# Optimization experiments

Measured on AMD Instinct MI355X. Metric: run time of the kernel, lower is better.

The kernel has to match this reference:

```python
import jax, jax.numpy as jnp
import numpy as np

DEGREE = 3
NUM_POINTS = 1024
EPS = 1e-5


def jacobi_kan(x, coeffs, a=1.0, b=1.0, degree=DEGREE):
    # x: (B, C_in, N) -> y: (B, C_out, N)
    t = jnp.tanh(jnp.transpose(x, (0, 2, 1)))  # (B, N, C_in)
    polys = [jnp.ones_like(t)]
    if degree > 0:
        polys.append((a - b + (a + b + 2.0) * t) / 2.0)
    for i in range(2, degree + 1):
        A = (2 * i + a + b - 1) * (2 * i + a + b) / (2 * i * (i + a + b))
        B = (2 * i + a + b - 1) * (a ** 2 - b ** 2) / (2 * i * (i + a + b) * (2 * i + a + b - 2))
        C = -2 * (i + a - 1) * (i + b - 1) * (2 * i + a + b) / (2 * i * (i + a + b) * (2 * i + a + b - 2))
        polys.append((A * t + B) * polys[-1] + C * polys[-2])
    jac = jnp.stack(polys, axis=-1)  # (B, N, C_in, D+1)
    return jnp.einsum('bnid,iod->bon', jac, coeffs)


def batchnorm(x):
    # x: (B, C, N); training-mode BN with batch stats, gamma=1, beta=0
    m = jnp.mean(x, axis=(0, 2), keepdims=True)
    v = jnp.var(x, axis=(0, 2), keepdims=True)
    return (x - m) * jax.lax.rsqrt(v + EPS)


def setup_inputs() -> dict:
    key = jax.random.key(0)
    ks = jax.random.split(key, 11)
    dims = [(2, 64), (64, 64), (64, 64), (64, 128), (128, 1024),
            (1088, 512), (512, 256), (256, 128), (128, 128), (128, 3)]
    inp = {"x": jax.random.normal(ks[0], (32, 2, NUM_POINTS), dtype=jnp.float32)}
    for idx, (i, o) in enumerate(dims):
        std = 1.0 / (i * (DEGREE + 1))
        inp[f"w{idx+1}"] = std * jax.random.normal(ks[idx + 1], (i, o, DEGREE + 1), dtype=jnp.float32)
    return inp


def reference(x, w1, w2, w3, w4, w5, w6, w7, w8, w9, w10):
    h = batchnorm(jacobi_kan(x, w1))
    h = batchnorm(jacobi_kan(h, w2))
    local_feature = h                                  # (B, 64, N)
    h = batchnorm(jacobi_kan(h, w3))
    h = batchnorm(jacobi_kan(h, w4))
    h = batchnorm(jacobi_kan(h, w5))                   # (B, 1024, N)
    gf = jnp.max(h, axis=2, keepdims=True)             # (B, 1024, 1)
    gf = jnp.broadcast_to(gf, (h.shape[0], h.shape[1], NUM_POINTS))
    h = jnp.concatenate([local_feature, gf], axis=1)   # (B, 1088, N)
    h = batchnorm(jacobi_kan(h, w6))
    h = batchnorm(jacobi_kan(h, w7))
    h = batchnorm(jacobi_kan(h, w8))
    h = batchnorm(jacobi_kan(h, w9))
    return jacobi_kan(h, w10)                          # (B, 3, N)
```

## Files before the change

### kernel.cpp

```cpp
#include <hip/hip_runtime.h>

#define BATCH 32
#define NPTS  1024
#define NTOT  (BATCH * NPTS)

typedef _Float16 half8  __attribute__((ext_vector_type(8)));
typedef _Float16 half4v __attribute__((ext_vector_type(4)));
typedef float    f32x4  __attribute__((ext_vector_type(4)));


__device__ __forceinline__ float fast_tanh(float x) {
  float ax = fabsf(x);
  float e  = __expf(-2.0f * ax);
  float t  = (1.0f - e) / (1.0f + e);
  return x < 0.0f ? -t : t;
}

__device__ __forceinline__ void jacobi4(float t, float& p0, float& p1, float& p2, float& p3) {
  float t2 = t * t;
  p0 = 1.0f;
  p1 = 2.0f * t;
  p2 = 3.75f * t2 - 0.75f;
  p3 = t * (7.0f * t2 - 3.0f);
}

__device__ __forceinline__ unsigned encf(float f) {
  unsigned b = __float_as_uint(f);
  return b ^ ((unsigned)((int)b >> 31) | 0x80000000u);
}
__device__ __forceinline__ float decf(unsigned u) {
  unsigned b = (u & 0x80000000u) ? (u ^ 0x80000000u) : ~u;
  return __uint_as_float(b);
}

__global__ void zero_ws(unsigned* __restrict__ p, int n) {
  int i = blockIdx.x * 256 + threadIdx.x;
  if (i < n) p[i] = 0u;
}

__global__ void conv_w16(const float* __restrict__ w, half8* __restrict__ wh,
                         int C_in, int C_out, int BN) {
  const int nslot = C_in >> 1;
  int tid = blockIdx.x * 256 + threadIdx.x;
  int oL = tid % BN;
  int r  = tid / BN;
  int s  = r % nslot;
  int ot = r / nslot;
  int i  = s << 1;
  int o  = ot * BN + oL;
  const float4 wa = *(const float4*)(w + (((size_t)i * C_out + o) << 2));
  const float4 wb = *(const float4*)(w + (((size_t)(i + 1) * C_out + o) << 2));
  half8 h;
  h[0] = (_Float16)(wa.x * 64.0f); h[1] = (_Float16)(wa.y * 64.0f);
  h[2] = (_Float16)(wa.z * 64.0f); h[3] = (_Float16)(wa.w * 64.0f);
  h[4] = (_Float16)(wb.x * 64.0f); h[5] = (_Float16)(wb.y * 64.0f);
  h[6] = (_Float16)(wb.z * 64.0f); h[7] = (_Float16)(wb.w * 64.0f);
  wh[tid] = h;
}

__global__ __launch_bounds__(256) void act_tanh(
    float* y, const float2* __restrict__ st, int C)
{
  size_t i = (((size_t)blockIdx.x << 8) + threadIdx.x) << 2;
  int c = (int)((i >> 10) % (unsigned)C);
  float2 s = st[c];
  float4 v = *(float4*)(y + i);
  v.x = fast_tanh((v.x - s.x) * s.y);
  v.y = fast_tanh((v.y - s.x) * s.y);
  v.z = fast_tanh((v.z - s.x) * s.y);
  v.w = fast_tanh((v.w - s.x) * s.y);
  *(float4*)(y + i) = v;
}

template<int NBW>
__global__ __launch_bounds__(NBW * 128, 2) void kan_mfma3(
    const float* __restrict__ T,
    const half8* __restrict__ wh,
    const float* __restrict__ bias,
    float*       __restrict__ out,
    float2*      __restrict__ spart,
    float*       __restrict__ stat_acc,
    unsigned*    __restrict__ max_acc,
    int C_in, int C_out)
{
  constexpr int BN = NBW * 64;
  const int nslot = C_in >> 1;
  __shared__ float sredS[BN][2], sredS2[BN][2], sredM[BN][2];

  const int t    = threadIdx.x;
  const int lane = t & 63;
  const int col  = lane & 15;
  const int quad = lane >> 4;
  const int wv   = t >> 6;
  const int wm   = wv & 1;
  const int wn   = wv >> 1;
  const int b    = blockIdx.x >> 3;
  const int n0   = (blockIdx.x & 7) << 7;
  const int o0   = blockIdx.y * BN;

  f32x4 acc[4][4];
#pragma unroll
  for (int i = 0; i < 4; ++i)
#pragma unroll
    for (int j = 0; j < 4; ++j)
#pragma unroll
      for (int k = 0; k < 4; ++k) acc[i][j][k] = 0.0f;

  const float* Tp = T + (((size_t)(b * C_in + (quad << 1))) << 10) + n0 + (wm << 6) + col;
  const half8* Bp = wh + (size_t)blockIdx.y * nslot * BN + (size_t)quad * BN + wn * 64 + col;

  for (int s4 = 0; s4 < nslot; s4 += 4) {
    float t0[4], t1[4];
    half8 bf[4];
#pragma unroll
    for (int f = 0; f < 4; ++f) {
      t0[f] = Tp[f << 4];
      t1[f] = Tp[(f << 4) + 1024];
      bf[f] = Bp[f << 4];
    }
    Tp += (size_t)8 << 10;
    Bp += (size_t)4 * BN;
    half8 af[4];
#pragma unroll
    for (int f = 0; f < 4; ++f) {
      float a = t0[f], c = t1[f];
      float as = a * a, cs = c * c;
      half8 h;
      h[0] = (_Float16)1.0f;
      h[1] = (_Float16)(a + a);
      h[2] = (_Float16)(3.75f * as - 0.75f);
      h[3] = (_Float16)(a * (7.0f * as - 3.0f));
      h[4] = (_Float16)1.0f;
      h[5] = (_Float16)(c + c);
      h[6] = (_Float16)(3.75f * cs - 0.75f);
      h[7] = (_Float16)(c * (7.0f * cs - 3.0f));
      af[f] = h;
    }
#pragma unroll
    for (int fm = 0; fm < 4; ++fm)
#pragma unroll
      for (int fn = 0; fn < 4; ++fn)
        acc[fm][fn] = __builtin_amdgcn_mfma_f32_16x16x32_f16(af[fm], bf[fn], acc[fm][fn], 0, 0, 0);
  }

  const float inv64 = 0.015625f;
#pragma unroll
  for (int fn = 0; fn < 4; ++fn) {
    const int cl = (wn << 6) + (fn << 4) + col;
    const int o  = o0 + cl;
    const float bb = bias ? bias[b * C_out + o] : 0.0f;
    float s = 0.f, s2 = 0.f, mx = -3.4e38f;
#pragma unroll
    for (int fm = 0; fm < 4; ++fm) {
      float v0 = acc[fm][fn][0] * inv64 + bb;
      float v1 = acc[fm][fn][1] * inv64 + bb;
      float v2 = acc[fm][fn][2] * inv64 + bb;
      float v3 = acc[fm][fn][3] * inv64 + bb;
      if (out) {
        *(float4*)(out + (((size_t)(b * C_out + o)) << 10) + n0 + (wm << 6) + (fm << 4) + (quad << 2)) =
            make_float4(v0, v1, v2, v3);
      }
      s  += v0 + v1 + v2 + v3;
      s2 += v0 * v0 + v1 * v1 + v2 * v2 + v3 * v3;
      mx  = fmaxf(fmaxf(v0, v1), fmaxf(fmaxf(v2, v3), mx));
    }
    s  += __shfl_down(s, 32);  s  += __shfl_down(s, 16);
    s2 += __shfl_down(s2, 32); s2 += __shfl_down(s2, 16);
    mx  = fmaxf(mx, __shfl_down(mx, 32)); mx = fmaxf(mx, __shfl_down(mx, 16));
    if (lane < 16) {
      sredS [cl][wm] = s;
      sredS2[cl][wm] = s2;
      sredM [cl][wm] = mx;
    }
  }
  __syncthreads();
  if (t < BN) {
    const int o = o0 + t;
    float s  = sredS [t][0] + sredS [t][1];
    float s2 = sredS2[t][0] + sredS2[t][1];
    if (out) {
      spart[(o << 8) + blockIdx.x] = make_float2(s, s2);
    } else {
      float mx = fmaxf(sredM[t][0], sredM[t][1]);
      atomicAdd(&stat_acc[o], s);
      atomicAdd(&stat_acc[C_out + o], s2);
      atomicMax(&max_acc[b * C_out + o], encf(mx));
    }
  }
}

template<int BM, int BN>
__global__ __launch_bounds__(256) void kan_gemm(
    const float*  __restrict__ in, const float2* __restrict__ stats,
    const float*  __restrict__ w, float* __restrict__ out,
    float2* __restrict__ spart, int C_in, int C_out)
{
  static_assert(BM * BN == 256 * 64, "8x8-per-thread tile requires BM*BN == 16384");
  constexpr int TM = BM / 8;
  constexpr int AE = 8 * BM / 256;
  constexpr int BE = 8 * BN / 256;
  __shared__ __align__(16) float As[32][BM];
  __shared__ __align__(16) float Bs[32][BN];

  const int t  = threadIdx.x;
  const int tpb = NPTS / BM;
  const int b  = blockIdx.x / tpb;
  const int n0 = (blockIdx.x % tpb) * BM;
  const int o0 = blockIdx.y * BN;
  const int tm = t % TM;
  const int to = t / TM;

  float acc[2][4][2][4];
#pragma unroll
  for (int a = 0; a < 2; ++a)
#pragma unroll
    for (int c = 0; c < 4; ++c)
#pragma unroll
      for (int d = 0; d < 2; ++d)
#pragma unroll
        for (int e = 0; e < 4; ++e) acc[a][c][d][e] = 0.0f;

  const int nch = (C_in + 7) >> 3;
  for (int ch = 0; ch < nch; ++ch) {
    const int i0 = ch << 3;
    __syncthreads();
#pragma unroll
    for (int r = 0; r < AE; ++r) {
      int e  = t + (r << 8);
      int il = e / BM, n = e % BM;
      int i  = i0 + il;
      float p0 = 0.f, p1 = 0.f, p2 = 0.f, p3 = 0.f;
      if (i < C_in) {
        float v = in[((size_t)(b * C_in + i) << 10) + n0 + n];
        if (stats) { float2 s = stats[i]; v = (v - s.x) * s.y; }
        jacobi4(fast_tanh(v), p0, p1, p2, p3);
      }
      As[(il << 2) + 0][n] = p0;
      As[(il << 2) + 1][n] = p1;
      As[(il << 2) + 2][n] = p2;
      As[(il << 2) + 3][n] = p3;
    }
#pragma unroll
    for (int r = 0; r < BE; ++r) {
      int e  = t + (r << 8);
      int il = e / BN, o = e % BN;
      int i  = i0 + il;
      float4 wv = make_float4(0.f, 0.f, 0.f, 0.f);
      if (i < C_in) wv = *(const float4*)(w + (((size_t)i * C_out + o0 + o) << 2));
      Bs[(il << 2) + 0][o] = wv.x;
      Bs[(il << 2) + 1][o] = wv.y;
      Bs[(il << 2) + 2][o] = wv.z;
      Bs[(il << 2) + 3][o] = wv.w;
    }
    __syncthreads();
#pragma unroll 8
    for (int k = 0; k < 32; ++k) {
      const float4 a0 = *(const float4*)&As[k][tm << 2];
      const float4 a1 = *(const float4*)&As[k][(BM / 2) + (tm << 2)];
      const float4 b0 = *(const float4*)&Bs[k][to << 2];
      const float4 b1 = *(const float4*)&Bs[k][(BN / 2) + (to << 2)];
      const float am[2][4] = {{a0.x, a0.y, a0.z, a0.w}, {a1.x, a1.y, a1.z, a1.w}};
      const float bo[2][4] = {{b0.x, b0.y, b0.z, b0.w}, {b1.x, b1.y, b1.z, b1.w}};
#pragma unroll
      for (int oh = 0; oh < 2; ++oh)
#pragma unroll
        for (int oj = 0; oj < 4; ++oj) {
          const float bv = bo[oh][oj];
#pragma unroll
          for (int mh = 0; mh < 2; ++mh)
#pragma unroll
            for (int mj = 0; mj < 4; ++mj)
              acc[oh][oj][mh][mj] = fmaf(bv, am[mh][mj], acc[oh][oj][mh][mj]);
        }
    }
  }

#pragma unroll
  for (int oh = 0; oh < 2; ++oh)
#pragma unroll
    for (int oj = 0; oj < 4; ++oj) {
      const int o = o0 + oh * (BN / 2) + (to << 2) + oj;
      float s = 0.f, s2 = 0.f;
#pragma unroll
      for (int mh = 0; mh < 2; ++mh) {
        float4 v = make_float4(acc[oh][oj][mh][0], acc[oh][oj][mh][1],
                               acc[oh][oj][mh][2], acc[oh][oj][mh][3]);
        *(float4*)(out + (((size_t)(b * C_out + o)) << 10) + n0 + mh * (BM / 2) + (tm << 2)) = v;
        s  += v.x + v.y + v.z + v.w;
        s2 += v.x * v.x + v.y * v.y + v.z * v.z + v.w * v.w;
      }
#pragma unroll
      for (int off = TM / 2; off > 0; off >>= 1) {
        s  += __shfl_down(s, off, TM);
        s2 += __shfl_down(s2, off, TM);
      }
      if (tm == 0) spart[(o << 8) + blockIdx.x] = make_float2(s, s2);
    }
}

__global__ __launch_bounds__(256) void bn_finalize2(
    const float2* __restrict__ spart, float2* __restrict__ stats, int C, int nxb)
{
  int c = blockIdx.x, t = threadIdx.x;
  float s = 0.f, s2 = 0.f;
  if (t < nxb) { float2 p = spart[(c << 8) + t]; s = p.x; s2 = p.y; }
#pragma unroll
  for (int off = 32; off > 0; off >>= 1) {
    s  += __shfl_down(s, off);
    s2 += __shfl_down(s2, off);
  }
  __shared__ float rs[4], rs2[4];
  int wid = t >> 6;
  if ((t & 63) == 0) { rs[wid] = s; rs2[wid] = s2; }
  __syncthreads();
  if (t == 0) {
    s  = rs[0] + rs[1] + rs[2] + rs[3];
    s2 = rs2[0] + rs2[1] + rs2[2] + rs2[3];
    float m   = s * (1.0f / NTOT);
    float var = s2 * (1.0f / NTOT) - m * m;
    stats[c] = make_float2(m, rsqrtf(var + 1e-5f));
  }
}

__global__ void bn_finalize(const float* __restrict__ stat_acc,
                            float2* __restrict__ stats, int C) {
  int c = blockIdx.x * 256 + threadIdx.x;
  if (c < C) {
    float m   = stat_acc[c] * (1.0f / NTOT);
    float var = stat_acc[C + c] * (1.0f / NTOT) - m * m;
    stats[c] = make_float2(m, rsqrtf(var + 1e-5f));
  }
}

__global__ __launch_bounds__(256) void pool_const6p(
    const unsigned* __restrict__ max_acc, const float2* __restrict__ stats5,
    const float* __restrict__ w6, float* __restrict__ cst)
{
  __shared__ __align__(16) float4 P[32][64];
  const int t  = threadIdx.x;
  const int ot = blockIdx.x;
  const int c0 = blockIdx.y << 6;
#pragma unroll
  for (int it = 0; it < 8; ++it) {
    int idx = t + (it << 8);
    int b = idx >> 6, cl = idx & 63;
    int c = c0 + cl;
    float mx = decf(max_acc[(b << 10) + c]);
    float2 s = stats5[c];
    float tt = fast_tanh((mx - s.x) * s.y);
    float p0, p1, p2, p3; jacobi4(tt, p0, p1, p2, p3);
    P[b][cl] = make_float4(p0, p1, p2, p3);
  }
  __syncthreads();
  const int oL = t & 63;
  const int bg = t >> 6;
  const int o  = (ot << 6) + oL;
  float acc[8];
#pragma unroll
  for (int i = 0; i < 8; ++i) acc[i] = 0.f;
  for (int cl = 0; cl < 64; ++cl) {
    const float4 wv = *(const float4*)(w6 + (((size_t)(64 + c0 + cl) * 512 + o) << 2));
#pragma unroll
    for (int bb = 0; bb < 8; ++bb) {
      float4 p = P[(bg << 3) + bb][cl];
      acc[bb] += p.x * wv.x + p.y * wv.y + p.z * wv.z + p.w * wv.w;
    }
  }
#pragma unroll
  for (int bb = 0; bb < 8; ++bb)
    atomicAdd(&cst[(((bg << 3) + bb) << 9) + o], acc[bb]);
}

__global__ __launch_bounds__(256) void kan_final(
    const float* __restrict__ in, const float2* __restrict__ stats,
    const float* __restrict__ w, float* __restrict__ out)
{
  int g = blockIdx.x * 256 + threadIdx.x;
  int b = g >> 10, n = g & 1023;
  float a0 = 0.f, a1 = 0.f, a2 = 0.f;
  for (int i = 0; i < 128; ++i) {
    float v = in[((size_t)(b * 128 + i) << 10) + n];
    float2 s = stats[i];
    float p0, p1, p2, p3; jacobi4(fast_tanh((v - s.x) * s.y), p0, p1, p2, p3);
    const float4 w0 = *(const float4*)(w + ((i * 3 + 0) << 2));
    const float4 w1 = *(const float4*)(w + ((i * 3 + 1) << 2));
    const float4 w2 = *(const float4*)(w + ((i * 3 + 2) << 2));
    a0 += p0 * w0.x + p1 * w0.y + p2 * w0.z + p3 * w0.w;
    a1 += p0 * w1.x + p1 * w1.y + p2 * w1.z + p3 * w1.w;
    a2 += p0 * w2.x + p1 * w2.y + p2 * w2.z + p3 * w2.w;
  }
  out[((b * 3 + 0) << 10) + n] = a0;
  out[((b * 3 + 1) << 10) + n] = a1;
  out[((b * 3 + 2) << 10) + n] = a2;
}

extern "C" void kernel_launch(void* const* d_in, const int* in_sizes, int n_in,
                              void* d_out, int out_size, void* d_ws, size_t ws_size,
                              hipStream_t stream) {
  const float* x   = (const float*)d_in[0];
  const float* w1  = (const float*)d_in[1];
  const float* w2  = (const float*)d_in[2];
  const float* w3  = (const float*)d_in[3];
  const float* w4  = (const float*)d_in[4];
  const float* w5  = (const float*)d_in[5];
  const float* w6  = (const float*)d_in[6];
  const float* w7  = (const float*)d_in[7];
  const float* w8  = (const float*)d_in[8];
  const float* w9  = (const float*)d_in[9];
  const float* w10 = (const float*)d_in[10];

  float* ws = (float*)d_ws;
  float*    stat_acc = ws + 0;
  unsigned* maxenc   = (unsigned*)(ws + 2048);
  float*    cst6     = ws + 34816;
  float2*   spart    = (float2*)(ws + 51200);
  float2*   stats1   = (float2*)(ws + 313344);
  float2*   stats2   = stats1 + 64;
  float2*   stats3   = stats2 + 64;
  float2*   stats4   = stats3 + 64;
  float2*   stats5   = stats4 + 128;
  float2*   stats6   = stats5 + 1024;
  float2*   stats7   = stats6 + 512;
  float2*   stats8   = stats7 + 256;
  float2*   stats9   = stats8 + 128;
  half8*    whbase = (half8*)(ws + 318464);
  half8*    h2 = whbase + 0;
  half8*    h3 = whbase + 2048;
  half8*    h4 = whbase + 4096;
  half8*    h5 = whbase + 8192;
  half8*    h6 = whbase + 73728;
  half8*    h7 = whbase + 90112;
  half8*    h8 = whbase + 155648;
  half8*    h9 = whbase + 172032;
  float* P   = ws + 1048576;
  float* yT2 = P;
  float* y6  = P + 2097152;
  float* y1  = P + 2097152;
  float* y3  = P + 4194304;
  float* y4  = P + 6291456;
  float* y8  = P + 2097152;
  float* y9  = P + 6291456;
  float* y7  = P + 18874368;

  dim3 blk(256);
  zero_ws<<<200, blk, 0, stream>>>((unsigned*)ws, 51200);
  conv_w16<<<8,   blk, 0, stream>>>(w2, h2, 64, 64, 64);
  conv_w16<<<8,   blk, 0, stream>>>(w3, h3, 64, 64, 64);
  conv_w16<<<16,  blk, 0, stream>>>(w4, h4, 64, 128, 128);
  conv_w16<<<256, blk, 0, stream>>>(w5, h5, 128, 1024, 128);
  conv_w16<<<64,  blk, 0, stream>>>(w6, h6, 64, 512, 128);
  conv_w16<<<256, blk, 0, stream>>>(w7, h7, 512, 256, 128);
  conv_w16<<<64,  blk, 0, stream>>>(w8, h8, 256, 128, 128);
  conv_w16<<<32,  blk, 0, stream>>>(w9, h9, 128, 128, 128);

  kan_gemm<256, 64><<<dim3(128, 1), blk, 0, stream>>>(x, nullptr, w1, y1, spart, 2, 64);
  bn_finalize2<<<64, blk, 0, stream>>>(spart, stats1, 64, 128);
  act_tanh<<<32 * 64, blk, 0, stream>>>(y1, stats1, 64);
  kan_mfma3<1><<<dim3(256, 1), 128, 0, stream>>>(y1, h2, nullptr, yT2, spart, nullptr, nullptr, 64, 64);
  bn_finalize2<<<64, blk, 0, stream>>>(spart, stats2, 64, 256);
  act_tanh<<<32 * 64, blk, 0, stream>>>(yT2, stats2, 64);
  kan_mfma3<1><<<dim3(256, 1), 128, 0, stream>>>(yT2, h3, nullptr, y3, spart, nullptr, nullptr, 64, 64);
  bn_finalize2<<<64, blk, 0, stream>>>(spart, stats3, 64, 256);
  act_tanh<<<32 * 64, blk, 0, stream>>>(y3, stats3, 64);
  kan_mfma3<2><<<dim3(256, 1), blk, 0, stream>>>(y3, h4, nullptr, y4, spart, nullptr, nullptr, 64, 128);
  bn_finalize2<<<128, blk, 0, stream>>>(spart, stats4, 128, 256);
  act_tanh<<<32 * 128, blk, 0, stream>>>(y4, stats4, 128);
  kan_mfma3<2><<<dim3(256, 8), blk, 0, stream>>>(y4, h5, nullptr, nullptr, nullptr, stat_acc, maxenc, 128, 1024);
  bn_finalize<<<4, blk, 0, stream>>>(stat_acc, stats5, 1024);
  pool_const6p<<<dim3(8, 16), blk, 0, stream>>>(maxenc, stats5, w6, cst6);
  kan_mfma3<2><<<dim3(256, 4), blk, 0, stream>>>(yT2, h6, cst6, y6, spart, nullptr, nullptr, 64, 512);
  bn_finalize2<<<512, blk, 0, stream>>>(spart, stats6, 512, 256);
  act_tanh<<<32 * 512, blk, 0, stream>>>(y6, stats6, 512);
  kan_mfma3<2><<<dim3(256, 2), blk, 0, stream>>>(y6, h7, nullptr, y7, spart, nullptr, nullptr, 512, 256);
  bn_finalize2<<<256, blk, 0, stream>>>(spart, stats7, 256, 256);
  act_tanh<<<32 * 256, blk, 0, stream>>>(y7, stats7, 256);
  kan_mfma3<2><<<dim3(256, 1), blk, 0, stream>>>(y7, h8, nullptr, y8, spart, nullptr, nullptr, 256, 128);
  bn_finalize2<<<128, blk, 0, stream>>>(spart, stats8, 128, 256);
  act_tanh<<<32 * 128, blk, 0, stream>>>(y8, stats8, 128);
  kan_mfma3<2><<<dim3(256, 1), blk, 0, stream>>>(y8, h9, nullptr, y9, spart, nullptr, nullptr, 128, 128);
  bn_finalize2<<<128, blk, 0, stream>>>(spart, stats9, 128, 256);
  kan_final<<<128, blk, 0, stream>>>(y9, stats9, w10, (float*)d_out);
}
```

Measured before the change: 422.6 us.

## Precompute fp16 Jacobi basis activations and fold P0 term into per-channel bias

Adds an act_poly3 pass that applies BN plus tanh and writes the P1..P3 Jacobi basis values as packed fp16 in a K-major layout. A new kan_mfma4 GEMM then streams those operands straight into MFMA instead of building them inside the inner loop. The constant P0=1 term is dropped from the GEMM and replaced by a precomputed column sum of w[:, :, 0] added as a bias, which cuts K by a quarter. The tradeoff is an extra fp16 activation buffer written and read per layer, and the new path only runs when the workspace is at least about 189 MB, otherwise the old path is kept.

New measurement: 606.4 us. 1.44x slower.

```diff
diff --git a/kernel.cpp b/kernel.cpp
--- a/kernel.cpp
+++ b/kernel.cpp
@@ -58,6 +58,43 @@
   wh[tid] = h;
 }
 
+__global__ __launch_bounds__(256) void conv_w16_3(
+    const float* __restrict__ w, half8* __restrict__ wh,
+    int C_in, int C_out, int BN)
+{
+  const int C8  = C_in >> 3;
+  const int nK8 = 3 * C8;
+  int tid = blockIdx.x * 256 + threadIdx.x;
+  int oL = tid % BN;
+  int r  = tid / BN;
+  int kg = r % nK8;
+  int ot = r / nK8;
+  int j  = kg / C8;
+  int cb = (kg - j * C8) << 3;
+  int o  = ot * BN + oL;
+  half8 h;
+#pragma unroll
+  for (int e = 0; e < 8; ++e) {
+    float v = w[(((size_t)(cb + e) * C_out + o) << 2) + (j + 1)];
+    h[e] = (_Float16)(v * 64.0f);
+  }
+  wh[tid] = h;
+}
+
+__global__ __launch_bounds__(256) void w0sum(
+    const float* __restrict__ w, float* __restrict__ s, int C_in, int C_out)
+{
+  __shared__ float r[3][64];
+  const int oL  = threadIdx.x & 63;
+  const int seg = threadIdx.x >> 6;
+  const int o   = (blockIdx.x << 6) + oL;
+  float a = 0.f;
+  for (int i = seg; i < C_in; i += 4) a += w[(((size_t)i * C_out + o) << 2)];
+  if (seg) r[seg - 1][oL] = a;
+  __syncthreads();
+  if (seg == 0) s[o] = a + r[0][oL] + r[1][oL] + r[2][oL];
+}
+
 __global__ __launch_bounds__(256) void act_tanh(
     float* y, const float2* __restrict__ st, int C)
 {
@@ -70,6 +107,56 @@
   v.z = fast_tanh((v.z - s.x) * s.y);
   v.w = fast_tanh((v.w - s.x) * s.y);
   *(float4*)(y + i) = v;
+}
+
+__global__ __launch_bounds__(256) void act_poly3(
+    const float* __restrict__ y, const float2* __restrict__ st,
+    half8* __restrict__ A, int C)
+{
+  const int C8 = C >> 3;
+  const int b  = blockIdx.x / C8;
+  const int cg = blockIdx.x - b * C8;
+  const int n  = threadIdx.x << 2;
+  const float* yp = y + (((size_t)(b * C + (cg << 3))) << 10) + n;
+  float q1[8][4], q2[8][4], q3[8][4];
+#pragma unroll
+  for (int e = 0; e < 8; ++e) {
+    float2 s = st[(cg << 3) + e];
+    float4 v = *(const float4*)(yp + ((size_t)e << 10));
+    float tv[4] = {v.x, v.y, v.z, v.w};
+#pragma unroll
+    for (int k = 0; k < 4; ++k) {
+      float tt = fast_tanh((tv[k] - s.x) * s.y);
+      float t2 = tt * tt;
+      q1[e][k] = tt + tt;
+      q2[e][k] = 3.75f * t2 - 0.75f;
+      q3[e][k] = tt * (7.0f * t2 - 3.0f);
+    }
+  }
+  half8* Ap = A + (((size_t)(b * 3 * C8 + cg)) << 10) + n;
+#pragma unroll
+  for (int k = 0; k < 4; ++k) {
+    half8 h;
+#pragma unroll
+    for (int e = 0; e < 8; ++e) h[e] = (_Float16)q1[e][k];
+    Ap[k] = h;
+  }
+  Ap += (size_t)C8 << 10;
+#pragma unroll
+  for (int k = 0; k < 4; ++k) {
+    half8 h;
+#pragma unroll
+    for (int e = 0; e < 8; ++e) h[e] = (_Float16)q2[e][k];
+    Ap[k] = h;
+  }
+  Ap += (size_t)C8 << 10;
+#pragma unroll
+  for (int k = 0; k < 4; ++k) {
+    half8 h;
+#pragma unroll
+    for (int e = 0; e < 8; ++e) h[e] = (_Float16)q3[e][k];
+    Ap[k] = h;
+  }
 }
 
 template<int NBW>
@@ -149,6 +236,105 @@
     const int cl = (wn << 6) + (fn << 4) + col;
     const int o  = o0 + cl;
     const float bb = bias ? bias[b * C_out + o] : 0.0f;
+    float s = 0.f, s2 = 0.f, mx = -3.4e38f;
+#pragma unroll
+    for (int fm = 0; fm < 4; ++fm) {
+      float v0 = acc[fm][fn][0] * inv64 + bb;
+      float v1 = acc[fm][fn][1] * inv64 + bb;
+      float v2 = acc[fm][fn][2] * inv64 + bb;
+      float v3 = acc[fm][fn][3] * inv64 + bb;
+      if (out) {
+        *(float4*)(out + (((size_t)(b * C_out + o)) << 10) + n0 + (wm << 6) + (fm << 4) + (quad << 2)) =
+            make_float4(v0, v1, v2, v3);
+      }
+      s  += v0 + v1 + v2 + v3;
+      s2 += v0 * v0 + v1 * v1 + v2 * v2 + v3 * v3;
+      mx  = fmaxf(fmaxf(v0, v1), fmaxf(fmaxf(v2, v3), mx));
+    }
+    s  += __shfl_down(s, 32);  s  += __shfl_down(s, 16);
+    s2 += __shfl_down(s2, 32); s2 += __shfl_down(s2, 16);
+    mx  = fmaxf(mx, __shfl_down(mx, 32)); mx = fmaxf(mx, __shfl_down(mx, 16));
+    if (lane < 16) {
+      sredS [cl][wm] = s;
+      sredS2[cl][wm] = s2;
+      sredM [cl][wm] = mx;
+    }
+  }
+  __syncthreads();
+  if (t < BN) {
+    const int o = o0 + t;
+    float s  = sredS [t][0] + sredS [t][1];
+    float s2 = sredS2[t][0] + sredS2[t][1];
+    if (out) {
+      spart[(o << 8) + blockIdx.x] = make_float2(s, s2);
+    } else {
+      float mx = fmaxf(sredM[t][0], sredM[t][1]);
+      atomicAdd(&stat_acc[o], s);
+      atomicAdd(&stat_acc[C_out + o], s2);
+      atomicMax(&max_acc[b * C_out + o], encf(mx));
+    }
+  }
+}
+
+template<int NBW>
+__global__ __launch_bounds__(NBW * 128, 2) void kan_mfma4(
+    const half8* __restrict__ A,
+    const half8* __restrict__ wh,
+    const float* __restrict__ w0s,
+    const float* __restrict__ bias,
+    float*       __restrict__ out,
+    float2*      __restrict__ spart,
+    float*       __restrict__ stat_acc,
+    unsigned*    __restrict__ max_acc,
+    int nK8, int C_out)
+{
+  constexpr int BN = NBW * 64;
+  __shared__ float sredS[BN][2], sredS2[BN][2], sredM[BN][2];
+
+  const int t    = threadIdx.x;
+  const int lane = t & 63;
+  const int col  = lane & 15;
+  const int quad = lane >> 4;
+  const int wv   = t >> 6;
+  const int wm   = wv & 1;
+  const int wn   = wv >> 1;
+  const int b    = blockIdx.x >> 3;
+  const int n0   = (blockIdx.x & 7) << 7;
+  const int o0   = blockIdx.y * BN;
+
+  f32x4 acc[4][4];
+#pragma unroll
+  for (int i = 0; i < 4; ++i)
+#pragma unroll
+    for (int j = 0; j < 4; ++j)
+#pragma unroll
+      for (int k = 0; k < 4; ++k) acc[i][j][k] = 0.0f;
+
+  const half8* Ap = A + (((size_t)b * nK8 + quad) << 10) + n0 + (wm << 6) + col;
+  const half8* Bp = wh + (size_t)blockIdx.y * nK8 * BN + (size_t)quad * BN + wn * 64 + col;
+
+  for (int g = 0; g < nK8; g += 4) {
+    half8 af[4], bf[4];
+#pragma unroll
+    for (int f = 0; f < 4; ++f) {
+      af[f] = Ap[f << 4];
+      bf[f] = Bp[f << 4];
+    }
+    Ap += (size_t)4 << 10;
+    Bp += (size_t)4 * BN;
+#pragma unroll
+    for (int fm = 0; fm < 4; ++fm)
+#pragma unroll
+      for (int fn = 0; fn < 4; ++fn)
+        acc[fm][fn] = __builtin_amdgcn_mfma_f32_16x16x32_f16(af[fm], bf[fn], acc[fm][fn], 0, 0, 0);
+  }
+
+  const float inv64 = 0.015625f;
+#pragma unroll
+  for (int fn = 0; fn < 4; ++fn) {
+    const int cl = (wn << 6) + (fn << 4) + col;
+    const int o  = o0 + cl;
+    const float bb = w0s[o] + (bias ? bias[b * C_out + o] : 0.0f);
     float s = 0.f, s2 = 0.f, mx = -3.4e38f;
 #pragma unroll
     for (int fm = 0; fm < 4; ++fm) {
@@ -410,74 +596,174 @@
   const float* w10 = (const float*)d_in[10];
 
   float* ws = (float*)d_ws;
-  float*    stat_acc = ws + 0;
-  unsigned* maxenc   = (unsigned*)(ws + 2048);
-  float*    cst6     = ws + 34816;
-  float2*   spart    = (float2*)(ws + 51200);
-  float2*   stats1   = (float2*)(ws + 313344);
-  float2*   stats2   = stats1 + 64;
-  float2*   stats3   = stats2 + 64;
-  float2*   stats4   = stats3 + 64;
-  float2*   stats5   = stats4 + 128;
-  float2*   stats6   = stats5 + 1024;
-  float2*   stats7   = stats6 + 512;
-  float2*   stats8   = stats7 + 256;
-  float2*   stats9   = stats8 + 128;
-  half8*    whbase = (half8*)(ws + 318464);
-  half8*    h2 = whbase + 0;
-  half8*    h3 = whbase + 2048;
-  half8*    h4 = whbase + 4096;
-  half8*    h5 = whbase + 8192;
-  half8*    h6 = whbase + 73728;
-  half8*    h7 = whbase + 90112;
-  half8*    h8 = whbase + 155648;
-  half8*    h9 = whbase + 172032;
-  float* P   = ws + 1048576;
-  float* yT2 = P;
-  float* y6  = P + 2097152;
-  float* y1  = P + 2097152;
-  float* y3  = P + 4194304;
-  float* y4  = P + 6291456;
-  float* y8  = P + 2097152;
-  float* y9  = P + 6291456;
-  float* y7  = P + 18874368;
-
   dim3 blk(256);
-  zero_ws<<<200, blk, 0, stream>>>((unsigned*)ws, 51200);
-  conv_w16<<<8,   blk, 0, stream>>>(w2, h2, 64, 64, 64);
-  conv_w16<<<8,   blk, 0, stream>>>(w3, h3, 64, 64, 64);
-  conv_w16<<<16,  blk, 0, stream>>>(w4, h4, 64, 128, 128);
-  conv_w16<<<256, blk, 0, stream>>>(w5, h5, 128, 1024, 128);
-  conv_w16<<<64,  blk, 0, stream>>>(w6, h6, 64, 512, 128);
-  conv_w16<<<256, blk, 0, stream>>>(w7, h7, 512, 256, 128);
-  conv_w16<<<64,  blk, 0, stream>>>(w8, h8, 256, 128, 128);
-  conv_w16<<<32,  blk, 0, stream>>>(w9, h9, 128, 128, 128);
-
-  kan_gemm<256, 64><<<dim3(128, 1), blk, 0, stream>>>(x, nullptr, w1, y1, spart, 2, 64);
-  bn_finalize2<<<64, blk, 0, stream>>>(spart, stats1, 64, 128);
-  act_tanh<<<32 * 64, blk, 0, stream>>>(y1, stats1, 64);
-  kan_mfma3<1><<<dim3(256, 1), 128, 0, stream>>>(y1, h2, nullptr, yT2, spart, nullptr, nullptr, 64, 64);
-  bn_finalize2<<<64, blk, 0, stream>>>(spart, stats2, 64, 256);
-  act_tanh<<<32 * 64, blk, 0, stream>>>(yT2, stats2, 64);
-  kan_mfma3<1><<<dim3(256, 1), 128, 0, stream>>>(yT2, h3, nullptr, y3, spart, nullptr, nullptr, 64, 64);
-  bn_finalize2<<<64, blk, 0, stream>>>(spart, stats3, 64, 256);
-  act_tanh<<<32 * 64, blk, 0, stream>>>(y3, stats3, 64);
-  kan_mfma3<2><<<dim3(256, 1), blk, 0, stream>>>(y3, h4, nullptr, y4, spart, nullptr, nullptr, 64, 128);
-  bn_finalize2<<<128, blk, 0, stream>>>(spart, stats4, 128, 256);
-  act_tanh<<<32 * 128, blk, 0, stream>>>(y4, stats4, 128);
-  kan_mfma3<2><<<dim3(256, 8), blk, 0, stream>>>(y4, h5, nullptr, nullptr, nullptr, stat_acc, maxenc, 128, 1024);
-  bn_finalize<<<4, blk, 0, stream>>>(stat_acc, stats5, 1024);
-  pool_const6p<<<dim3(8, 16), blk, 0, stream>>>(maxenc, stats5, w6, cst6);
-  kan_mfma3<2><<<dim3(256, 4), blk, 0, stream>>>(yT2, h6, cst6, y6, spart, nullptr, nullptr, 64, 512);
-  bn_finalize2<<<512, blk, 0, stream>>>(spart, stats6, 512, 256);
-  act_tanh<<<32 * 512, blk, 0, stream>>>(y6, stats6, 512);
-  kan_mfma3<2><<<dim3(256, 2), blk, 0, stream>>>(y6, h7, nullptr, y7, spart, nullptr, nullptr, 512, 256);
-  bn_finalize2<<<256, blk, 0, stream>>>(spart, stats7, 256, 256);
-  act_tanh<<<32 * 256, blk, 0, stream>>>(y7, stats7, 256);
-  kan_mfma3<2><<<dim3(256, 1), blk, 0, stream>>>(y7, h8, nullptr, y8, spart, nullptr, nullptr, 256, 128);
-  bn_finalize2<<<128, blk, 0, stream>>>(spart, stats8, 128, 256);
-  act_tanh<<<32 * 128, blk, 0, stream>>>(y8, stats8, 128);
-  kan_mfma3<2><<<dim3(256, 1), blk, 0, stream>>>(y8, h9, nullptr, y9, spart, nullptr, nullptr, 128, 128);
-  bn_finalize2<<<128, blk, 0, stream>>>(spart, stats9, 128, 256);
-  kan_final<<<128, blk, 0, stream>>>(y9, stats9, w10, (float*)d_out);
-}
+
+  if (ws_size >= 188743680ULL) {
+    float*    stat_acc = ws + 0;
+    unsigned* maxenc   = (unsigned*)(ws + 2048);
+    float*    cst6     = ws + 34816;
+    float2*   spart    = (float2*)(ws + 51200);
+    float2*   stats1   = (float2*)(ws + 313344);
+    float2*   stats2   = stats1 + 64;
+    float2*   stats3   = stats2 + 64;
+    float2*   stats4   = stats3 + 64;
+    float2*   stats5   = stats4 + 128;
+    float2*   stats6   = stats5 + 1024;
+    float2*   stats7   = stats6 + 512;
+    float2*   stats8   = stats7 + 256;
+    float2*   stats9   = stats8 + 128;
+    float*    w0s2 = ws + 318080;
+    float*    w0s3 = w0s2 + 64;
+    float*    w0s4 = w0s3 + 64;
+    float*    w0s5 = w0s4 + 128;
+    float*    w0s6 = w0s5 + 1024;
+    float*    w0s7 = w0s6 + 512;
+    float*    w0s8 = w0s7 + 256;
+    float*    w0s9 = w0s8 + 128;
+    half8*    whb = (half8*)(ws + 320384);
+    half8*    h2 = whb + 0;
+    half8*    h3 = whb + 1536;
+    half8*    h4 = whb + 3072;
+    half8*    h5 = whb + 6144;
+    half8*    h6 = whb + 55296;
+    half8*    h7 = whb + 67584;
+    half8*    h8 = whb + 116736;
+    half8*    h9 = whb + 129024;
+    const size_t MF = 1048576;
+    float* P  = ws + 2 * MF;
+    float* A2 = P;
+    float* y1 = P + 3 * MF;
+    float* A1 = P + 5 * MF;
+    float* y2 = P + 3 * MF;
+    float* y3 = P + 5 * MF;
+    float* A3 = P + 7 * MF;
+    float* y4 = P + 3 * MF;
+    float* A4 = P + 7 * MF;
+    float* y6 = P + 3 * MF;
+    float* A6 = P + 19 * MF;
+    float* y7 = P;
+    float* A7 = P + 8 * MF;
+    float* y8 = P;
+    float* A8 = P + 4 * MF;
+    float* y9 = P;
+
+    zero_ws<<<200, blk, 0, stream>>>((unsigned*)ws, 51200);
+    conv_w16_3<<<6,   blk, 0, stream>>>(w2, h2, 64, 64, 64);
+    conv_w16_3<<<6,   blk, 0, stream>>>(w3, h3, 64, 64, 64);
+    conv_w16_3<<<12,  blk, 0, stream>>>(w4, h4, 64, 128, 128);
+    conv_w16_3<<<192, blk, 0, stream>>>(w5, h5, 128, 1024, 128);
+    conv_w16_3<<<48,  blk, 0, stream>>>(w6, h6, 64, 512, 128);
+    conv_w16_3<<<192, blk, 0, stream>>>(w7, h7, 512, 256, 128);
+    conv_w16_3<<<48,  blk, 0, stream>>>(w8, h8, 256, 128, 128);
+    conv_w16_3<<<24,  blk, 0, stream>>>(w9, h9, 128, 128, 128);
+    w0sum<<<1,  blk, 0, stream>>>(w2, w0s2, 64, 64);
+    w0sum<<<1,  blk, 0, stream>>>(w3, w0s3, 64, 64);
+    w0sum<<<2,  blk, 0, stream>>>(w4, w0s4, 64, 128);
+    w0sum<<<16, blk, 0, stream>>>(w5, w0s5, 128, 1024);
+    w0sum<<<8,  blk, 0, stream>>>(w6, w0s6, 64, 512);
+    w0sum<<<4,  blk, 0, stream>>>(w7, w0s7, 512, 256);
+    w0sum<<<2,  blk, 0, stream>>>(w8, w0s8, 256, 128);
+    w0sum<<<2,  blk, 0, stream>>>(w9, w0s9, 128, 128);
+
+    kan_gemm<256, 64><<<dim3(128, 1), blk, 0, stream>>>(x, nullptr, w1, y1, spart, 2, 64);
+    bn_finalize2<<<64, blk, 0, stream>>>(spart, stats1, 64, 128);
+    act_poly3<<<256, blk, 0, stream>>>(y1, stats1, (half8*)A1, 64);
+    kan_mfma4<1><<<dim3(256, 1), 128, 0, stream>>>((half8*)A1, h2, w0s2, nullptr, y2, spart, nullptr, nullptr, 24, 64);
+    bn_finalize2<<<64, blk, 0, stream>>>(spart, stats2, 64, 256);
+    act_poly3<<<256, blk, 0, stream>>>(y2, stats2, (half8*)A2, 64);
+    kan_mfma4<1><<<dim3(256, 1), 128, 0, stream>>>((half8*)A2, h3, w0s3, nullptr, y3, spart, nullptr, nullptr, 24, 64);
+    bn_finalize2<<<64, blk, 0, stream>>>(spart, stats3, 64, 256);
+    act_poly3<<<256, blk, 0, stream>>>(y3, stats3, (half8*)A3, 64);
+    kan_mfma4<2><<<dim3(256, 1), blk, 0, stream>>>((half8*)A3, h4, w0s4, nullptr, y4, spart, nullptr, nullptr, 24, 128);
+    bn_finalize2<<<128, blk, 0, stream>>>(spart, stats4, 128, 256);
+    act_poly3<<<512, blk, 0, stream>>>(y4, stats4, (half8*)A4, 128);
+    kan_mfma4<2><<<dim3(256, 8), blk, 0, stream>>>((half8*)A4, h5, w0s5, nullptr, nullptr, nullptr, stat_acc, maxenc, 48, 1024);
+    bn_finalize<<<4, blk, 0, stream>>>(stat_acc, stats5, 1024);
+    pool_const6p<<<dim3(8, 16), blk, 0, stream>>>(maxenc, stats5, w6, cst6);
+    kan_mfma4<2><<<dim3(256, 4), blk, 0, stream>>>((half8*)A2, h6, w0s6, cst6, y6, spart, nullptr, nullptr, 24, 512);
+    bn_finalize2<<<512, blk, 0, stream>>>(spart, stats6, 512, 256);
+    act_poly3<<<2048, blk, 0, stream>>>(y6, stats6, (half8*)A6, 512);
+    kan_mfma4<2><<<dim3(256, 2), blk, 0, stream>>>((half8*)A6, h7, w0s7, nullptr, y7, spart, nullptr, nullptr, 192, 256);
+    bn_finalize2<<<256, blk, 0, stream>>>(spart, stats7, 256, 256);
+    act_poly3<<<1024, blk, 0, stream>>>(y7, stats7, (half8*)A7, 256);
+    kan_mfma4<2><<<dim3(256, 1), blk, 0, stream>>>((half8*)A7, h8, w0s8, nullptr, y8, spart, nullptr, nullptr, 96, 128);
+    bn_finalize2<<<128, blk, 0, stream>>>(spart, stats8, 128, 256);
+    act_poly3<<<512, blk, 0, stream>>>(y8, stats8, (half8*)A8, 128);
+    kan_mfma4<2><<<dim3(256, 1), blk, 0, stream>>>((half8*)A8, h9, w0s9, nullptr, y9, spart, nullptr, nullptr, 48, 128);
+    bn_finalize2<<<128, blk, 0, stream>>>(spart, stats9, 128, 256);
+    kan_final<<<128, blk, 0, stream>>>(y9, stats9, w10, (float*)d_out);
+    return;
+  }
+
+  {
+    float*    stat_acc = ws + 0;
+    unsigned* maxenc   = (unsigned*)(ws + 2048);
+    float*    cst6     = ws + 34816;
+    float2*   spart    = (float2*)(ws + 51200);
+    float2*   stats1   = (float2*)(ws + 313344);
+    float2*   stats2   = stats1 + 64;
+    float2*   stats3   = stats2 + 64;
+    float2*   stats4   = stats3 + 64;
+    float2*   stats5   = stats4 + 128;
+    float2*   stats6   = stats5 + 1024;
+    float2*   stats7   = stats6 + 512;
+    float2*   stats8   = stats7 + 256;
+    float2*   stats9   = stats8 + 128;
+    half8*    whbase = (half8*)(ws + 318464);
+    half8*    h2 = whbase + 0;
+    half8*    h3 = whbase + 2048;
+    half8*    h4 = whbase + 4096;
+    half8*    h5 = whbase + 8192;
+    half8*    h6 = whbase + 73728;
+    half8*    h7 = whbase + 90112;
+    half8*    h8 = whbase + 155648;
+    half8*    h9 = whbase + 172032;
+    float* P   = ws + 1048576;
+    float* yT2 = P;
+    float* y6  = P + 2097152;
+    float* y1  = P + 2097152;
+    float* y3  = P + 4194304;
+    float* y4  = P + 6291456;
+    float* y8  = P + 2097152;
+    float* y9  = P + 6291456;
+    float* y7  = P + 18874368;
+
+    zero_ws<<<200, blk, 0, stream>>>((unsigned*)ws, 51200);
+    conv_w16<<<8,   blk, 0, stream>>>(w2, h2, 64, 64, 64);
+    conv_w16<<<8,   blk, 0, stream>>>(w3, h3, 64, 64, 64);
+    conv_w16<<<16,  blk, 0, stream>>>(w4, h4, 64, 128, 128);
+    conv_w16<<<256, blk, 0, stream>>>(w5, h5, 128, 1024, 128);
+    conv_w16<<<64,  blk, 0, stream>>>(w6, h6, 64, 512, 128);
+    conv_w16<<<256, blk, 0, stream>>>(w7, h7, 512, 256, 128);
+    conv_w16<<<64,  blk, 0, stream>>>(w8, h8, 256, 128, 128);
+    conv_w16<<<32,  blk, 0, stream>>>(w9, h9, 128, 128, 128);
+
+    kan_gemm<256, 64><<<dim3(128, 1), blk, 0, stream>>>(x, nullptr, w1, y1, spart, 2, 64);
+    bn_finalize2<<<64, blk, 0, stream>>>(spart, stats1, 64, 128);
+    act_tanh<<<32 * 64, blk, 0, stream>>>(y1, stats1, 64);
+    kan_mfma3<1><<<dim3(256, 1), 128, 0, stream>>>(y1, h2, nullptr, yT2, spart, nullptr, nullptr, 64, 64);
+    bn_finalize2<<<64, blk, 0, stream>>>(spart, stats2, 64, 256);
+    act_tanh<<<32 * 64, blk, 0, stream>>>(yT2, stats2, 64);
+    kan_mfma3<1><<<dim3(256, 1), 128, 0, stream>>>(yT2, h3, nullptr, y3, spart, nullptr, nullptr, 64, 64);
+    bn_finalize2<<<64, blk, 0, stream>>>(spart, stats3, 64, 256);
+    act_tanh<<<32 * 64, blk, 0, stream>>>(y3, stats3, 64);
+    kan_mfma3<2><<<dim3(256, 1), blk, 0, stream>>>(y3, h4, nullptr, y4, spart, nullptr, nullptr, 64, 128);
+    bn_finalize2<<<128, blk, 0, stream>>>(spart, stats4, 128, 256);
+    act_tanh<<<32 * 128, blk, 0, stream>>>(y4, stats4, 128);
+    kan_mfma3<2><<<dim3(256, 8), blk, 0, stream>>>(y4, h5, nullptr, nullptr, nullptr, stat_acc, maxenc, 128, 1024);
+    bn_finalize<<<4, blk, 0, stream>>>(stat_acc, stats5, 1024);
+    pool_const6p<<<dim3(8, 16), blk, 0, stream>>>(maxenc, stats5, w6, cst6);
+    kan_mfma3<2><<<dim3(256, 4), blk, 0, stream>>>(yT2, h6, cst6, y6, spart, nullptr, nullptr, 64, 512);
+    bn_finalize2<<<512, blk, 0, stream>>>(spart, stats6, 512, 256);
+    act_tanh<<<32 * 512, blk, 0, stream>>>(y6, stats6, 512);
+    kan_mfma3<2><<<dim3(256, 2), blk, 0, stream>>>(y6, h7, nullptr, y7, spart, nullptr, nullptr, 512, 256);
+    bn_finalize2<<<256, blk, 0, stream>>>(spart, stats7, 256, 256);
+    act_tanh<<<32 * 256, blk, 0, stream>>>(y7, stats7, 256);
+    kan_mfma3<2><<<dim3(256, 1), blk, 0, stream>>>(y7, h8, nullptr, y8, spart, nullptr, nullptr, 256, 128);
+    bn_finalize2<<<128, blk, 0, stream>>>(spart, stats8, 128, 256);
+    act_tanh<<<32 * 128, blk, 0, stream>>>(y8, stats8, 128);
+    kan_mfma3<2><<<dim3(256, 1), blk, 0, stream>>>(y8, h9, nullptr, y9, spart, nullptr, nullptr, 128, 128);
+    bn_finalize2<<<128, blk, 0, stream>>>(spart, stats9, 128, 256);
+    kan_final<<<128, blk, 0, stream>>>(y9, stats9, w10, (float*)d_out);
+  }
+}
```

## Store tanh activations as packed fp16 pairs and double-buffer GEMM loads

Applied to the files above, without the earlier changes.

The activation kernel now writes tanh outputs as packed half2 pairs interleaved by channel pair, in a separate buffer rather than in place. The MFMA kernel reads these halved-size operands, computes the Jacobi basis with packed fp16 arithmetic, and software-pipelines its loads with two register buffers. The workspace buffer layout is reorganised to match. This cuts activation-read bandwidth and the conversion ALU work in the GEMMs, at the cost of computing the polynomial basis in fp16, which lowers precision, and more registers for the double buffer.

New measurement: 382.6 us. -9.5%, faster.

```diff
diff --git a/kernel.cpp b/kernel.cpp
--- a/kernel.cpp
+++ b/kernel.cpp
@@ -5,7 +5,7 @@
 #define NTOT  (BATCH * NPTS)
 
 typedef _Float16 half8  __attribute__((ext_vector_type(8)));
-typedef _Float16 half4v __attribute__((ext_vector_type(4)));
+typedef _Float16 half2v __attribute__((ext_vector_type(2)));
 typedef float    f32x4  __attribute__((ext_vector_type(4)));
 
 
@@ -58,23 +58,36 @@
   wh[tid] = h;
 }
 
-__global__ __launch_bounds__(256) void act_tanh(
-    float* y, const float2* __restrict__ st, int C)
+__global__ __launch_bounds__(256) void act_tanh16(
+    const float* __restrict__ y, const float2* __restrict__ st,
+    unsigned* __restrict__ T16, int C)
 {
-  size_t i = (((size_t)blockIdx.x << 8) + threadIdx.x) << 2;
-  int c = (int)((i >> 10) % (unsigned)C);
-  float2 s = st[c];
-  float4 v = *(float4*)(y + i);
-  v.x = fast_tanh((v.x - s.x) * s.y);
-  v.y = fast_tanh((v.y - s.x) * s.y);
-  v.z = fast_tanh((v.z - s.x) * s.y);
-  v.w = fast_tanh((v.w - s.x) * s.y);
-  *(float4*)(y + i) = v;
+  const int nslot = C >> 1;
+  const int b  = blockIdx.x / nslot;
+  const int s  = blockIdx.x - b * nslot;
+  const int n  = threadIdx.x << 2;
+  const float* yp = y + (((size_t)(b * C + (s << 1))) << 10) + n;
+  const float2 s0 = st[(s << 1)];
+  const float2 s1 = st[(s << 1) + 1];
+  float4 v0 = *(const float4*)yp;
+  float4 v1 = *(const float4*)(yp + 1024);
+  float a0[4] = {v0.x, v0.y, v0.z, v0.w};
+  float a1[4] = {v1.x, v1.y, v1.z, v1.w};
+  unsigned r[4];
+#pragma unroll
+  for (int k = 0; k < 4; ++k) {
+    _Float16 h0 = (_Float16)fast_tanh((a0[k] - s0.x) * s0.y);
+    _Float16 h1 = (_Float16)fast_tanh((a1[k] - s1.x) * s1.y);
+    unsigned lo = (unsigned)__builtin_bit_cast(unsigned short, h0);
+    unsigned hi = (unsigned)__builtin_bit_cast(unsigned short, h1);
+    r[k] = lo | (hi << 16);
+  }
+  *(uint4*)(T16 + (((size_t)(b * nslot + s)) << 10) + n) = make_uint4(r[0], r[1], r[2], r[3]);
 }
 
 template<int NBW>
-__global__ __launch_bounds__(NBW * 128, 2) void kan_mfma3(
-    const float* __restrict__ T,
+__global__ __launch_bounds__(NBW * 128, 2) void kan_mfma7(
+    const unsigned* __restrict__ T16,
     const half8* __restrict__ wh,
     const float* __restrict__ bias,
     float*       __restrict__ out,
@@ -106,42 +119,61 @@
 #pragma unroll
       for (int k = 0; k < 4; ++k) acc[i][j][k] = 0.0f;
 
-  const float* Tp = T + (((size_t)(b * C_in + (quad << 1))) << 10) + n0 + (wm << 6) + col;
-  const half8* Bp = wh + (size_t)blockIdx.y * nslot * BN + (size_t)quad * BN + wn * 64 + col;
-
-  for (int s4 = 0; s4 < nslot; s4 += 4) {
-    float t0[4], t1[4];
-    half8 bf[4];
-#pragma unroll
-    for (int f = 0; f < 4; ++f) {
-      t0[f] = Tp[f << 4];
-      t1[f] = Tp[(f << 4) + 1024];
-      bf[f] = Bp[f << 4];
-    }
-    Tp += (size_t)8 << 10;
-    Bp += (size_t)4 * BN;
-    half8 af[4];
-#pragma unroll
-    for (int f = 0; f < 4; ++f) {
-      float a = t0[f], c = t1[f];
-      float as = a * a, cs = c * c;
-      half8 h;
-      h[0] = (_Float16)1.0f;
-      h[1] = (_Float16)(a + a);
-      h[2] = (_Float16)(3.75f * as - 0.75f);
-      h[3] = (_Float16)(a * (7.0f * as - 3.0f));
-      h[4] = (_Float16)1.0f;
-      h[5] = (_Float16)(c + c);
-      h[6] = (_Float16)(3.75f * cs - 0.75f);
-      h[7] = (_Float16)(c * (7.0f * cs - 3.0f));
-      af[f] = h;
-    }
-#pragma unroll
-    for (int fm = 0; fm < 4; ++fm)
-#pragma unroll
-      for (int fn = 0; fn < 4; ++fn)
-        acc[fm][fn] = __builtin_amdgcn_mfma_f32_16x16x32_f16(af[fm], bf[fn], acc[fm][fn], 0, 0, 0);
-  }
+  const unsigned* Tp = T16 + (((size_t)(b * nslot + quad)) << 10) + n0 + (wm << 6) + col;
+  const half8*    Bp = wh + (size_t)blockIdx.y * nslot * BN + (size_t)quad * BN + wn * 64 + col;
+
+  const half2v c375  = {(_Float16)3.75f,  (_Float16)3.75f};
+  const half2v cm075 = {(_Float16)-0.75f, (_Float16)-0.75f};
+  const half2v c70   = {(_Float16)7.0f,   (_Float16)7.0f};
+  const half2v cm30  = {(_Float16)-3.0f,  (_Float16)-3.0f};
+
+#define KLOAD(TTR, BFR, J) do {                                            \
+    const unsigned* tp_ = Tp + (((size_t)(unsigned)(J)) << 12);            \
+    const half8*    bp_ = Bp + (size_t)(unsigned)(J) * (BN << 2);          \
+    TTR[0] = tp_[0];  TTR[1] = tp_[16];                                    \
+    TTR[2] = tp_[32]; TTR[3] = tp_[48];                                    \
+    BFR[0] = bp_[0];  BFR[1] = bp_[16];                                    \
+    BFR[2] = bp_[32]; BFR[3] = bp_[48];                                    \
+  } while (0)
+
+#define KSTEP(TTR, BFR) do {                                               \
+    half8 af_[4];                                                          \
+    _Pragma("unroll")                                                      \
+    for (int fm_ = 0; fm_ < 4; ++fm_) {                                    \
+      half2v tt = __builtin_bit_cast(half2v, TTR[fm_]);                    \
+      half2v t2 = tt * tt;                                                 \
+      half2v q1 = tt + tt;                                                 \
+      half2v q2 = t2 * c375 + cm075;                                       \
+      half2v q3 = tt * (t2 * c70 + cm30);                                  \
+      half8 h;                                                             \
+      h[0] = (_Float16)1.0f; h[1] = q1[0]; h[2] = q2[0]; h[3] = q3[0];     \
+      h[4] = (_Float16)1.0f; h[5] = q1[1]; h[6] = q2[1]; h[7] = q3[1];     \
+      af_[fm_] = h;                                                        \
+    }                                                                      \
+    _Pragma("unroll")                                                      \
+    for (int fm_ = 0; fm_ < 4; ++fm_) {                                    \
+      _Pragma("unroll")                                                    \
+      for (int fn_ = 0; fn_ < 4; ++fn_)                                    \
+        acc[fm_][fn_] = __builtin_amdgcn_mfma_f32_16x16x32_f16(            \
+            af_[fm_], BFR[fn_], acc[fm_][fn_], 0, 0, 0);                   \
+    }                                                                      \
+  } while (0)
+
+  const int nIt = nslot >> 2;
+  unsigned ttA[4], ttB[4];
+  half8    bfA[4], bfB[4];
+  KLOAD(ttA, bfA, 0);
+  KLOAD(ttB, bfB, 1);
+  int it = 0;
+  for (; it + 3 < nIt; it += 2) {
+    KSTEP(ttA, bfA); KLOAD(ttA, bfA, it + 2);
+    KSTEP(ttB, bfB); KLOAD(ttB, bfB, it + 3);
+  }
+  KSTEP(ttA, bfA);
+  KSTEP(ttB, bfB);
+
+#undef KLOAD
+#undef KSTEP
 
   const float inv64 = 0.015625f;
 #pragma unroll
@@ -432,15 +464,23 @@
   half8*    h7 = whbase + 90112;
   half8*    h8 = whbase + 155648;
   half8*    h9 = whbase + 172032;
-  float* P   = ws + 1048576;
-  float* yT2 = P;
-  float* y6  = P + 2097152;
-  float* y1  = P + 2097152;
-  float* y3  = P + 4194304;
-  float* y4  = P + 6291456;
-  float* y8  = P + 2097152;
-  float* y9  = P + 6291456;
-  float* y7  = P + 18874368;
+  const size_t MF = 1048576;
+  float*    P   = ws + MF;
+  unsigned* T2  = (unsigned*)(P + 0 * MF);
+  float*    y1  = P + 1 * MF;
+  unsigned* T1  = (unsigned*)(P + 3 * MF);
+  float*    y2  = P + 1 * MF;
+  float*    y3  = P + 1 * MF;
+  unsigned* T3  = (unsigned*)(P + 3 * MF);
+  float*    y4  = P + 4 * MF;
+  unsigned* T4  = (unsigned*)(P + 1 * MF);
+  float*    y6  = P + 3 * MF;
+  unsigned* T6  = (unsigned*)(P + 19 * MF);
+  float*    y7  = P + 0 * MF;
+  unsigned* T7  = (unsigned*)(P + 8 * MF);
+  float*    y8  = P + 0 * MF;
+  unsigned* T8  = (unsigned*)(P + 4 * MF);
+  float*    y9  = P + 12 * MF;
 
   dim3 blk(256);
   zero_ws<<<200, blk, 0, stream>>>((unsigned*)ws, 51200);
@@ -455,29 +495,29 @@
 
   kan_gemm<256, 64><<<dim3(128, 1), blk, 0, stream>>>(x, nullptr, w1, y1, spart, 2, 64);
   bn_finalize2<<<64, blk, 0, stream>>>(spart, stats1, 64, 128);
-  act_tanh<<<32 * 64, blk, 0, stream>>>(y1, stats1, 64);
-  kan_mfma3<1><<<dim3(256, 1), 128, 0, stream>>>(y1, h2, nullptr, yT2, spart, nullptr, nullptr, 64, 64);
+  act_tanh16<<<32 * 32, blk, 0, stream>>>(y1, stats1, T1, 64);
+  kan_mfma7<1><<<dim3(256, 1), 128, 0, stream>>>(T1, h2, nullptr, y2, spart, nullptr, nullptr, 64, 64);
   bn_finalize2<<<64, blk, 0, stream>>>(spart, stats2, 64, 256);
-  act_tanh<<<32 * 64, blk, 0, stream>>>(yT2, stats2, 64);
-  kan_mfma3<1><<<dim3(256, 1), 128, 0, stream>>>(yT2, h3, nullptr, y3, spart, nullptr, nullptr, 64, 64);
+  act_tanh16<<<32 * 32, blk, 0, stream>>>(y2, stats2, T2, 64);
+  kan_mfma7<1><<<dim3(256, 1), 128, 0, stream>>>(T2, h3, nullptr, y3, spart, nullptr, nullptr, 64, 64);
   bn_finalize2<<<64, blk, 0, stream>>>(spart, stats3, 64, 256);
-  act_tanh<<<32 * 64, blk, 0, stream>>>(y3, stats3, 64);
-  kan_mfma3<2><<<dim3(256, 1), blk, 0, stream>>>(y3, h4, nullptr, y4, spart, nullptr, nullptr, 64, 128);
+  act_tanh16<<<32 * 32, blk, 0, stream>>>(y3, stats3, T3, 64);
+  kan_mfma7<2><<<dim3(256, 1), blk, 0, stream>>>(T3, h4, nullptr, y4, spart, nullptr, nullptr, 64, 128);
   bn_finalize2<<<128, blk, 0, stream>>>(spart, stats4, 128, 256);
-  act_tanh<<<32 * 128, blk, 0, stream>>>(y4, stats4, 128);
-  kan_mfma3<2><<<dim3(256, 8), blk, 0, stream>>>(y4, h5, nullptr, nullptr, nullptr, stat_acc, maxenc, 128, 1024);
+  act_tanh16<<<32 * 64, blk, 0, stream>>>(y4, stats4, T4, 128);
+  kan_mfma7<2><<<dim3(256, 8), blk, 0, stream>>>(T4, h5, nullptr, nullptr, nullptr, stat_acc, maxenc, 128, 1024);
   bn_finalize<<<4, blk, 0, stream>>>(stat_acc, stats5, 1024);
   pool_const6p<<<dim3(8, 16), blk, 0, stream>>>(maxenc, stats5, w6, cst6);
-  kan_mfma3<2><<<dim3(256, 4), blk, 0, stream>>>(yT2, h6, cst6, y6, spart, nullptr, nullptr, 64, 512);
+  kan_mfma7<2><<<dim3(256, 4), blk, 0, stream>>>(T2, h6, cst6, y6, spart, nullptr, nullptr, 64, 512);
   bn_finalize2<<<512, blk, 0, stream>>>(spart, stats6, 512, 256);
-  act_tanh<<<32 * 512, blk, 0, stream>>>(y6, stats6, 512);
-  kan_mfma3<2><<<dim3(256, 2), blk, 0, stream>>>(y6, h7, nullptr, y7, spart, nullptr, nullptr, 512, 256);
+  act_tanh16<<<32 * 256, blk, 0, stream>>>(y6, stats6, T6, 512);
+  kan_mfma7<2><<<dim3(256, 2), blk, 0, stream>>>(T6, h7, nullptr, y7, spart, nullptr, nullptr, 512, 256);
   bn_finalize2<<<256, blk, 0, stream>>>(spart, stats7, 256, 256);
-  act_tanh<<<32 * 256, blk, 0, stream>>>(y7, stats7, 256);
-  kan_mfma3<2><<<dim3(256, 1), blk, 0, stream>>>(y7, h8, nullptr, y8, spart, nullptr, nullptr, 256, 128);
+  act_tanh16<<<32 * 128, blk, 0, stream>>>(y7, stats7, T7, 256);
+  kan_mfma7<2><<<dim3(256, 1), blk, 0, stream>>>(T7, h8, nullptr, y8, spart, nullptr, nullptr, 256, 128);
   bn_finalize2<<<128, blk, 0, stream>>>(spart, stats8, 128, 256);
-  act_tanh<<<32 * 128, blk, 0, stream>>>(y8, stats8, 128);
-  kan_mfma3<2><<<dim3(256, 1), blk, 0, stream>>>(y8, h9, nullptr, y9, spart, nullptr, nullptr, 128, 128);
+  act_tanh16<<<32 * 64, blk, 0, stream>>>(y8, stats8, T8, 128);
+  kan_mfma7<2><<<dim3(256, 1), blk, 0, stream>>>(T8, h9, nullptr, y9, spart, nullptr, nullptr, 128, 128);
   bn_finalize2<<<128, blk, 0, stream>>>(spart, stats9, 128, 256);
   kan_final<<<128, blk, 0, stream>>>(y9, stats9, w10, (float*)d_out);
 }
```
